# Kernel optimization log

Hardware: AMD Instinct MI355X
Metric: run time of the kernel (lower is better)

Reference implementation:

```python
import jax, jax.numpy as jnp
import numpy as np

HEADS = 8
DIM_HEAD = 32
GROUPS = 8
EPS = 1e-5


def setup_inputs() -> dict:
    key = jax.random.key(0)
    k0, k1, k2 = jax.random.split(key, 3)
    dim = 256
    inner = HEADS * DIM_HEAD  # 256
    x = jax.random.normal(k0, (1, dim, 16, 16, 16), dtype=jnp.float32)
    gn_weight = jnp.ones((dim,), dtype=jnp.float32)
    gn_bias = jnp.zeros((dim,), dtype=jnp.float32)
    w_qkv = jax.random.normal(k1, (3 * inner, dim), dtype=jnp.float32) * 0.02
    w_out = jax.random.normal(k2, (dim, inner), dtype=jnp.float32) * 0.02
    b_out = jnp.zeros((dim,), dtype=jnp.float32)
    return {"x": x, "gn_weight": gn_weight, "gn_bias": gn_bias,
            "w_qkv": w_qkv, "w_out": w_out, "b_out": b_out}


def reference(x, gn_weight, gn_bias, w_qkv, w_out, b_out):
    b, c, d, h, w = x.shape
    n = d * h * w  # tokens

    # --- GroupNorm(8, c) with affine ---
    xg = x.reshape(b, GROUPS, c // GROUPS, n)
    mean = xg.mean(axis=(2, 3), keepdims=True)
    var = xg.var(axis=(2, 3), keepdims=True)
    xn = ((xg - mean) * jax.lax.rsqrt(var + EPS)).reshape(b, c, n)
    xn = xn * gn_weight[:, None] + gn_bias[:, None]

    # --- 1x1 Conv3d QKV projection (no bias) ---
    qkv = jnp.einsum('bcn,oc->bon', xn, w_qkv)              # (b, 3*H*dh, n)
    qkv = qkv.reshape(b, 3, HEADS, DIM_HEAD, n)
    q, k, v = qkv[:, 0], qkv[:, 1], qkv[:, 2]               # each (b, H, dh, n)

    # --- naive softmax attention over n = d*h*w tokens ---
    scale = DIM_HEAD ** (-0.5)
    sim = jnp.einsum('bhdi,bhdj->bhij', q, k) * scale       # (b, H, n, n)
    attn = jax.nn.softmax(sim, axis=-1)
    out = jnp.einsum('bhij,bhdj->bhdi', attn, v)            # (b, H, dh, n)
    out = out.reshape(b, HEADS * DIM_HEAD, n)

    # --- 1x1 Conv3d output projection (with bias) ---
    y = jnp.einsum('bcn,oc->bon', out, w_out) + b_out[:, None]
    return y.reshape(b, c, d, h, w)
```

## Files before the change

### kernel.cpp

```cpp
#include <hip/hip_runtime.h>
#include <hip/hip_bf16.h>
#include <math.h>


typedef __attribute__((ext_vector_type(8))) short bf16x8;
typedef __attribute__((ext_vector_type(4))) short bf16x4;
typedef __attribute__((ext_vector_type(4))) float f32x4;
typedef __attribute__((ext_vector_type(4))) unsigned short u16x4;

__device__ inline unsigned short f2bf(float f) {
  __hip_bfloat16 h = __float2bfloat16(f);
  return *reinterpret_cast<unsigned short*>(&h);
}

__device__ inline bf16x4 pack4_bf(float p0, float p1, float p2, float p3) {
  float2 a, b;
  a.x = p0; a.y = p1; b.x = p2; b.y = p3;
  __hip_bfloat162 lo = __float22bfloat162_rn(a);
  __hip_bfloat162 hi = __float22bfloat162_rn(b);
  union U { __hip_bfloat162 h2[2]; bf16x4 v; } u;
  u.h2[0] = lo; u.h2[1] = hi;
  return u.v;
}

__global__ __launch_bounds__(256) void xt_gn_kernel(const float* __restrict__ x,
                                                    unsigned short* __restrict__ xTb,
                                                    float2* __restrict__ psum2) {
  __shared__ float tile[64][65];
  __shared__ float red[4][4];
  int nb = blockIdx.x * 64, cb = blockIdx.y * 64;
  int tn = threadIdx.x & 63, t4 = threadIdx.x >> 6;
  float slo = 0.f, qlo = 0.f, shi = 0.f, qhi = 0.f;
#pragma unroll
  for (int i = 0; i < 16; ++i) {
    int cc = t4 + i * 4;
    float v = x[(size_t)(cb + cc) * 4096 + nb + tn];
    tile[cc][tn] = v;
    if (i < 8) { slo += v; qlo += v * v; } else { shi += v; qhi += v * v; }
  }
#pragma unroll
  for (int off = 32; off > 0; off >>= 1) {
    slo += __shfl_down(slo, off); qlo += __shfl_down(qlo, off);
    shi += __shfl_down(shi, off); qhi += __shfl_down(qhi, off);
  }
  if ((threadIdx.x & 63) == 0) {
    red[t4][0] = slo; red[t4][1] = qlo; red[t4][2] = shi; red[t4][3] = qhi;
  }
  __syncthreads();
  if (threadIdx.x == 0) {
    float a = (red[0][0] + red[1][0]) + (red[2][0] + red[3][0]);
    float b = (red[0][1] + red[1][1]) + (red[2][1] + red[3][1]);
    psum2[(blockIdx.y * 2) * 64 + blockIdx.x] = make_float2(a, b);
  } else if (threadIdx.x == 64) {
    float a = (red[0][2] + red[1][2]) + (red[2][2] + red[3][2]);
    float b = (red[0][3] + red[1][3]) + (red[2][3] + red[3][3]);
    psum2[(blockIdx.y * 2 + 1) * 64 + blockIdx.x] = make_float2(a, b);
  }
#pragma unroll
  for (int i = 0; i < 16; ++i) {
    int nn = t4 + i * 4;
    xTb[(size_t)(nb + nn) * 256 + cb + tn] = f2bf(tile[tn][nn]);
  }
}

__global__ __launch_bounds__(256) void fold_all_kernel(const float* __restrict__ w_qkv,
                                                       const float* __restrict__ gnw,
                                                       const float* __restrict__ gnb,
                                                       const float2* __restrict__ psum2,
                                                       const float* __restrict__ w_out,
                                                       unsigned short* __restrict__ w2b,
                                                       float* __restrict__ bias0,
                                                       unsigned short* __restrict__ w_outb) {
  int bid = blockIdx.x;
  int t = threadIdx.x;
  if (bid >= 192) {
    int i = ((bid - 192) * 256 + t) * 4;
    float4 v = *(const float4*)(w_out + i);
    u16x4 o;
    o[0] = f2bf(v.x); o[1] = f2bf(v.y); o[2] = f2bf(v.z); o[3] = f2bf(v.w);
    *(u16x4*)(w_outb + i) = o;
    return;
  }
  __shared__ float sm[8], sr[8];
  __shared__ float s_al[256], s_be[256];
  {
    int g = t >> 5, ii = t & 31;
    float2 p0 = psum2[g * 64 + ii];
    float2 p1 = psum2[g * 64 + 32 + ii];
    float s = p0.x + p1.x, q = p0.y + p1.y;
#pragma unroll
    for (int off = 16; off > 0; off >>= 1) {
      s += __shfl_xor(s, off);
      q += __shfl_xor(q, off);
    }
    if (ii == 0) {
      float mean = s * (1.f / 131072.f);
      float var = q * (1.f / 131072.f) - mean * mean;
      sm[g] = mean;
      sr[g] = rsqrtf(var + 1e-5f);
    }
  }
  __syncthreads();
  {
    int c = t, gg = c >> 5;
    float mean = sm[gg], rstd = sr[gg];
    float al = rstd * gnw[c];
    s_al[c] = al;
    s_be[c] = gnb[c] - mean * al;
  }
  __syncthreads();
  int w = t >> 6, lane = t & 63;
  int row = bid * 4 + w;
  float4 v = *(const float4*)(w_qkv + row * 256 + lane * 4);
  int c0 = lane * 4;
  float part = (v.x * s_be[c0] + v.y * s_be[c0 + 1]) +
               (v.z * s_be[c0 + 2] + v.w * s_be[c0 + 3]);
  u16x4 o;
  o[0] = f2bf(v.x * s_al[c0]);
  o[1] = f2bf(v.y * s_al[c0 + 1]);
  o[2] = f2bf(v.z * s_al[c0 + 2]);
  o[3] = f2bf(v.w * s_al[c0 + 3]);
  *(u16x4*)(w2b + row * 256 + c0) = o;
#pragma unroll
  for (int off = 32; off > 0; off >>= 1) part += __shfl_down(part, off);
  if (lane == 0) bias0[row] = part;
}

__global__ __launch_bounds__(256) void gemm_qkv_mfma(const unsigned short* __restrict__ w2b,
                                                     const unsigned short* __restrict__ xTb,
                                                     const float* __restrict__ bias0,
                                                     unsigned short* __restrict__ qt,
                                                     unsigned short* __restrict__ ktb,
                                                     unsigned short* __restrict__ v16) {
  const int nb = blockIdx.x, mb = blockIdx.y;
  const int t = threadIdx.x;
  const int w = t >> 6, lane = t & 63;
  const int c = lane & 15, g = lane >> 4;
  const int m0 = mb * 64 + w * 16;
  const int n0 = nb * 64;
  const f32x4 zero4 = {0.f, 0.f, 0.f, 0.f};

  const unsigned short* ap = w2b + (size_t)(m0 + c) * 256 + g * 8;
  bf16x8 af[8];
#pragma unroll
  for (int ks = 0; ks < 8; ++ks) af[ks] = *(const bf16x8*)(ap + ks * 32);

  f32x4 acc[4] = {zero4, zero4, zero4, zero4};
  const unsigned short* bp = xTb + (size_t)(n0 + c) * 256 + g * 8;
#pragma unroll
  for (int half = 0; half < 2; ++half) {
    bf16x8 bf[4][4];
#pragma unroll
    for (int nt = 0; nt < 4; ++nt)
#pragma unroll
      for (int k2 = 0; k2 < 4; ++k2)
        bf[nt][k2] = *(const bf16x8*)(bp + (size_t)nt * 4096 + half * 128 + k2 * 32);
#pragma unroll
    for (int k2 = 0; k2 < 4; ++k2)
#pragma unroll
      for (int nt = 0; nt < 4; ++nt)
        acc[nt] = __builtin_amdgcn_mfma_f32_16x16x32_bf16(af[half * 4 + k2], bf[nt][k2],
                                                          acc[nt], 0, 0, 0);
  }

  const int o0 = m0 + g * 4;
  const int t3 = o0 >> 8;
  const int h = (o0 >> 5) & 7;
  const int d0 = o0 & 31;
  float b4[4];
#pragma unroll
  for (int r = 0; r < 4; ++r) b4[r] = bias0[o0 + r];
  const float qs = 0.17677669529663687f * 1.4426950408889634f;
#pragma unroll
  for (int nt = 0; nt < 4; ++nt) {
    int n = n0 + nt * 16 + c;
    if (t3 == 0) {
      u16x4 v;
#pragma unroll
      for (int r = 0; r < 4; ++r) v[r] = f2bf((acc[nt][r] + b4[r]) * qs);
      *(u16x4*)(qt + (size_t)(h * 4096 + n) * 32 + d0) = v;
    } else if (t3 == 1) {
      u16x4 v;
#pragma unroll
      for (int r = 0; r < 4; ++r) v[r] = f2bf(acc[nt][r] + b4[r]);
      *(u16x4*)(ktb + (size_t)(h * 4096 + n) * 32 + d0) = v;
    } else {
#pragma unroll
      for (int r = 0; r < 4; ++r)
        v16[(size_t)((h * 256 + (n >> 4)) * 32 + d0 + r) * 16 + (n & 15)] =
            f2bf(acc[nt][r] + b4[r]);
    }
  }
}

__global__ __launch_bounds__(512) void attn_mfma_kernel(const unsigned short* __restrict__ qt,
                                                        const unsigned short* __restrict__ ktb,
                                                        const unsigned short* __restrict__ v16,
                                                        unsigned short* __restrict__ outTb) {
  const int b = blockIdx.x;
  const int h = b & 7;
  const int i0 = (b >> 3) * 64;
  const int t = threadIdx.x;
  const int w = t >> 6;
  const int lane = t & 63;
  const int c = lane & 15;
  const int g = lane >> 4;
  const f32x4 zero4 = {0.f, 0.f, 0.f, 0.f};

  const unsigned short* qb = qt + (size_t)h * 131072 + (size_t)(i0 + c) * 32 + g * 8;
  bf16x8 qf[4];
#pragma unroll
  for (int it = 0; it < 4; ++it) qf[it] = *(const bf16x8*)(qb + it * 512);

  const unsigned short* kp = ktb + (size_t)h * 131072 + (size_t)(w * 512 + c) * 32 + g * 8;
  const unsigned short* vp = v16 + (size_t)((h * 256 + w * 32) * 32 + c) * 16 + g * 4;

  float l[4] = {0.f, 0.f, 0.f, 0.f};
  f32x4 oacc[4][2];
#pragma unroll
  for (int it = 0; it < 4; ++it) {
    oacc[it][0] = zero4;
    oacc[it][1] = zero4;
  }

  bf16x8 kf[4], kn[4];
#pragma unroll
  for (int js = 0; js < 4; ++js) kf[js] = *(const bf16x8*)(kp + js * 512);

#pragma unroll 1
  for (int jt = 0; jt < 8; ++jt) {
    bf16x4 vf[2][4];
#pragma unroll
    for (int dh = 0; dh < 2; ++dh)
#pragma unroll
      for (int js = 0; js < 4; ++js)
        vf[dh][js] = *(const bf16x4*)(vp + (jt * 4 + js) * 512 + dh * 256);
    int jn = (jt < 7) ? jt + 1 : 7;
#pragma unroll
    for (int js = 0; js < 4; ++js)
      kn[js] = *(const bf16x8*)(kp + jn * 2048 + js * 512);

#pragma unroll
    for (int it = 0; it < 4; ++it) {
      f32x4 st[4];
      __builtin_amdgcn_s_setprio(1);
#pragma unroll
      for (int js = 0; js < 4; ++js)
        st[js] = __builtin_amdgcn_mfma_f32_16x16x32_bf16(kf[js], qf[it], zero4, 0, 0, 0);
      __builtin_amdgcn_s_setprio(0);
      bf16x4 pb[4];
      float lsum = 0.f;
#pragma unroll
      for (int js = 0; js < 4; ++js) {
        float p0 = __builtin_amdgcn_exp2f(st[js][0]);
        float p1 = __builtin_amdgcn_exp2f(st[js][1]);
        float p2 = __builtin_amdgcn_exp2f(st[js][2]);
        float p3 = __builtin_amdgcn_exp2f(st[js][3]);
        lsum += (p0 + p1) + (p2 + p3);
        pb[js] = pack4_bf(p0, p1, p2, p3);
      }
      l[it] += lsum;
      __builtin_amdgcn_s_setprio(1);
#pragma unroll
      for (int js = 0; js < 4; ++js) {
        oacc[it][0] = __builtin_amdgcn_mfma_f32_16x16x16bf16_1k(vf[0][js], pb[js], oacc[it][0], 0, 0, 0);
        oacc[it][1] = __builtin_amdgcn_mfma_f32_16x16x16bf16_1k(vf[1][js], pb[js], oacc[it][1], 0, 0, 0);
      }
      __builtin_amdgcn_s_setprio(0);
    }
#pragma unroll
    for (int js = 0; js < 4; ++js) kf[js] = kn[js];
  }

  __shared__ float lds_o[8][4][2][4][4][17];
  __shared__ float lds_l[8][4][16];
#pragma unroll
  for (int it = 0; it < 4; ++it) {
    float lv = l[it];
    lv += __shfl_xor(lv, 16);
    lv += __shfl_xor(lv, 32);
    if (g == 0) lds_l[w][it][c] = lv;
#pragma unroll
    for (int dh = 0; dh < 2; ++dh)
#pragma unroll
      for (int r = 0; r < 4; ++r)
        lds_o[w][it][dh][g][r][c] = oacc[it][dh][r];
  }
  __syncthreads();
  {
    const int it = w & 3;
    const int dh = w >> 2;
    float L = ((lds_l[0][it][c] + lds_l[1][it][c]) + (lds_l[2][it][c] + lds_l[3][it][c])) +
              ((lds_l[4][it][c] + lds_l[5][it][c]) + (lds_l[6][it][c] + lds_l[7][it][c]));
    float inv = 1.f / L;
    u16x4 o;
#pragma unroll
    for (int r = 0; r < 4; ++r) {
      float v = ((lds_o[0][it][dh][g][r][c] + lds_o[1][it][dh][g][r][c]) +
                 (lds_o[2][it][dh][g][r][c] + lds_o[3][it][dh][g][r][c])) +
                ((lds_o[4][it][dh][g][r][c] + lds_o[5][it][dh][g][r][c]) +
                 (lds_o[6][it][dh][g][r][c] + lds_o[7][it][dh][g][r][c]));
      o[r] = f2bf(v * inv);
    }
    *(u16x4*)(outTb + (size_t)(i0 + it * 16 + c) * 256 + h * 32 + dh * 16 + g * 4) = o;
  }
}

__global__ __launch_bounds__(256) void gemm_out_mfma(const unsigned short* __restrict__ w_outb,
                                                     const unsigned short* __restrict__ outTb,
                                                     const float* __restrict__ bias,
                                                     float* __restrict__ y) {
  const int nb = blockIdx.x, mb = blockIdx.y;
  const int t = threadIdx.x;
  const int w = t >> 6, lane = t & 63;
  const int c = lane & 15, g = lane >> 4;
  const int m0 = mb * 64 + w * 16;
  const int n0 = nb * 64;
  const f32x4 zero4 = {0.f, 0.f, 0.f, 0.f};

  const unsigned short* ap = w_outb + (size_t)(m0 + c) * 256 + g * 8;
  bf16x8 af[8];
#pragma unroll
  for (int ks = 0; ks < 8; ++ks) af[ks] = *(const bf16x8*)(ap + ks * 32);

  f32x4 acc[4] = {zero4, zero4, zero4, zero4};
  const unsigned short* bp = outTb + (size_t)(n0 + c) * 256 + g * 8;
#pragma unroll
  for (int half = 0; half < 2; ++half) {
    bf16x8 bf[4][4];
#pragma unroll
    for (int nt = 0; nt < 4; ++nt)
#pragma unroll
      for (int k2 = 0; k2 < 4; ++k2)
        bf[nt][k2] = *(const bf16x8*)(bp + (size_t)nt * 4096 + half * 128 + k2 * 32);
#pragma unroll
    for (int k2 = 0; k2 < 4; ++k2)
#pragma unroll
      for (int nt = 0; nt < 4; ++nt)
        acc[nt] = __builtin_amdgcn_mfma_f32_16x16x32_bf16(af[half * 4 + k2], bf[nt][k2],
                                                          acc[nt], 0, 0, 0);
  }

  const int o0 = m0 + g * 4;
  float b4[4];
#pragma unroll
  for (int r = 0; r < 4; ++r) b4[r] = bias[o0 + r];
#pragma unroll
  for (int nt = 0; nt < 4; ++nt) {
    int n = n0 + nt * 16 + c;
#pragma unroll
    for (int r = 0; r < 4; ++r)
      y[(size_t)(o0 + r) * 4096 + n] = acc[nt][r] + b4[r];
  }
}

extern "C" void kernel_launch(void* const* d_in, const int* in_sizes, int n_in,
                              void* d_out, int out_size, void* d_ws, size_t ws_size,
                              hipStream_t stream) {
  const float* x = (const float*)d_in[0];
  const float* gnw = (const float*)d_in[1];
  const float* gnb = (const float*)d_in[2];
  const float* w_qkv = (const float*)d_in[3];
  const float* w_out = (const float*)d_in[4];
  const float* b_out = (const float*)d_in[5];
  float* ws = (float*)d_ws;

  float2* psum2 = (float2*)ws;
  float* bias0 = ws + 1088;
  unsigned short* w2b = (unsigned short*)(ws + 2048);
  unsigned short* w_outb = w2b + 196608;
  unsigned short* xTb = w_outb + 65536;
  unsigned short* qt = xTb + 1048576;
  unsigned short* ktb = qt + 1048576;
  unsigned short* v16 = ktb + 1048576;
  unsigned short* outTb = v16 + 1048576;
  float* y = (float*)d_out;

  hipLaunchKernelGGL(xt_gn_kernel, dim3(64, 4), dim3(256), 0, stream, x, xTb, psum2);
  hipLaunchKernelGGL(fold_all_kernel, dim3(256), dim3(256), 0, stream, w_qkv, gnw, gnb,
                     psum2, w_out, w2b, bias0, w_outb);
  hipLaunchKernelGGL(gemm_qkv_mfma, dim3(64, 12), dim3(256), 0, stream, w2b, xTb, bias0, qt, ktb, v16);
  hipLaunchKernelGGL(attn_mfma_kernel, dim3(512), dim3(512), 0, stream, qt, ktb, v16, outTb);
  hipLaunchKernelGGL(gemm_out_mfma, dim3(64, 4), dim3(256), 0, stream, w_outb, outTb, b_out, y);
}
```

Measured before the change: 69.78 us.

## Stage K/V tiles in LDS with async double buffering, split attention by queries

The attention kernel now gives each wave its own 16 query rows and has every wave walk all keys. K and V tiles are staged into swizzled LDS double buffers with global_load_lds, so all 8 waves share one copy of each tile instead of each wave loading its own key slice from global memory. This removes the cross-wave LDS reduction of partial outputs and row sums at the end. V is written by the QKV GEMM in a plain transposed [h][d][n] layout to suit the LDS staging. The grid halves to 256 blocks of 128 queries, which lowers parallelism and adds a block barrier per key tile.

After: 82.39 us. 1.18x slower.

```diff
diff --git a/kernel.cpp b/kernel.cpp
--- a/kernel.cpp
+++ b/kernel.cpp
@@ -21,6 +21,12 @@
   union U { __hip_bfloat162 h2[2]; bf16x4 v; } u;
   u.h2[0] = lo; u.h2[1] = hi;
   return u.v;
+}
+
+__device__ inline void gld_lds16(const void* g, void* l) {
+  __builtin_amdgcn_global_load_lds(
+      (const __attribute__((address_space(1))) void*)g,
+      (__attribute__((address_space(3))) void*)l, 16, 0, 0);
 }
 
 __global__ __launch_bounds__(256) void xt_gn_kernel(const float* __restrict__ x,
@@ -131,7 +137,7 @@
                                                      const float* __restrict__ bias0,
                                                      unsigned short* __restrict__ qt,
                                                      unsigned short* __restrict__ ktb,
-                                                     unsigned short* __restrict__ v16) {
+                                                     unsigned short* __restrict__ vT) {
   const int nb = blockIdx.x, mb = blockIdx.y;
   const int t = threadIdx.x;
   const int w = t >> 6, lane = t & 63;
@@ -187,19 +193,18 @@
     } else {
 #pragma unroll
       for (int r = 0; r < 4; ++r)
-        v16[(size_t)((h * 256 + (n >> 4)) * 32 + d0 + r) * 16 + (n & 15)] =
-            f2bf(acc[nt][r] + b4[r]);
+        vT[(size_t)(h * 32 + d0 + r) * 4096 + n] = f2bf(acc[nt][r] + b4[r]);
     }
   }
 }
 
 __global__ __launch_bounds__(512) void attn_mfma_kernel(const unsigned short* __restrict__ qt,
                                                         const unsigned short* __restrict__ ktb,
-                                                        const unsigned short* __restrict__ v16,
+                                                        const unsigned short* __restrict__ vT,
                                                         unsigned short* __restrict__ outTb) {
   const int b = blockIdx.x;
   const int h = b & 7;
-  const int i0 = (b >> 3) * 64;
+  const int i0 = (b >> 3) * 128;
   const int t = threadIdx.x;
   const int w = t >> 6;
   const int lane = t & 63;
@@ -207,102 +212,87 @@
   const int g = lane >> 4;
   const f32x4 zero4 = {0.f, 0.f, 0.f, 0.f};
 
-  const unsigned short* qb = qt + (size_t)h * 131072 + (size_t)(i0 + c) * 32 + g * 8;
-  bf16x8 qf[4];
-#pragma unroll
-  for (int it = 0; it < 4; ++it) qf[it] = *(const bf16x8*)(qb + it * 512);
-
-  const unsigned short* kp = ktb + (size_t)h * 131072 + (size_t)(w * 512 + c) * 32 + g * 8;
-  const unsigned short* vp = v16 + (size_t)((h * 256 + w * 32) * 32 + c) * 16 + g * 4;
-
-  float l[4] = {0.f, 0.f, 0.f, 0.f};
-  f32x4 oacc[4][2];
-#pragma unroll
-  for (int it = 0; it < 4; ++it) {
-    oacc[it][0] = zero4;
-    oacc[it][1] = zero4;
-  }
-
-  bf16x8 kf[4], kn[4];
-#pragma unroll
-  for (int js = 0; js < 4; ++js) kf[js] = *(const bf16x8*)(kp + js * 512);
-
+  __shared__ __align__(16) unsigned short kbuf[2][4096];
+  __shared__ __align__(16) unsigned short vbuf[2][4096];
+
+  const bf16x8 qf = *(const bf16x8*)(qt + (size_t)h * 131072 +
+                                     (size_t)(i0 + w * 16 + c) * 32 + g * 8);
+
+  const char* kbase = (const char*)(ktb + (size_t)h * 131072);
+  const char* vbase = (const char*)(vT + (size_t)h * 131072);
+  const int ksrc = (t * 16) ^ (((t >> 3) & 3) << 4);
+  const int vd = t >> 4;
+  const int vsrc = ((t & 15) * 16) ^ ((vd & 7) << 4);
+  char* kdst0 = (char*)&kbuf[0][0] + w * 1024;
+  char* vdst0 = (char*)&vbuf[0][0] + w * 1024;
+
+  const int krd_base = c * 64 + g * 16;
+  const int kswz = ((c >> 1) & 3) << 4;
+  const int vswz = (c & 7) << 4;
+
+  f32x4 oacc[2] = {zero4, zero4};
+  float l = 0.f;
+
+#define STAGE(bb, tt)                                                     \
+  do {                                                                    \
+    gld_lds16(kbase + (size_t)(tt) * 8192 + ksrc, kdst0 + (bb) * 8192);   \
+    gld_lds16(vbase + (size_t)vd * 8192 + (size_t)(tt) * 256 + vsrc,      \
+              vdst0 + (bb) * 8192);                                       \
+  } while (0)
+
+  STAGE(0, 0);
+  __syncthreads();
+
+  int cur = 0;
 #pragma unroll 1
-  for (int jt = 0; jt < 8; ++jt) {
-    bf16x4 vf[2][4];
+  for (int tt = 0; tt < 32; ++tt) {
+    if (tt < 31) STAGE(cur ^ 1, tt + 1);
+
+    const char* kb = (const char*)&kbuf[cur][0];
+    const char* vb = (const char*)&vbuf[cur][0];
+
+    f32x4 st[8];
+#pragma unroll
+    for (int js = 0; js < 8; ++js) {
+      bf16x8 kf = *(const bf16x8*)(kb + ((js * 1024 + krd_base) ^ kswz));
+      st[js] = __builtin_amdgcn_mfma_f32_16x16x32_bf16(kf, qf, zero4, 0, 0, 0);
+    }
+
+    bf16x4 pb[8];
+    float lsum = 0.f;
+#pragma unroll
+    for (int js = 0; js < 8; ++js) {
+      float p0 = __builtin_amdgcn_exp2f(st[js][0]);
+      float p1 = __builtin_amdgcn_exp2f(st[js][1]);
+      float p2 = __builtin_amdgcn_exp2f(st[js][2]);
+      float p3 = __builtin_amdgcn_exp2f(st[js][3]);
+      lsum += (p0 + p1) + (p2 + p3);
+      pb[js] = pack4_bf(p0, p1, p2, p3);
+    }
+    l += lsum;
+
 #pragma unroll
     for (int dh = 0; dh < 2; ++dh)
 #pragma unroll
-      for (int js = 0; js < 4; ++js)
-        vf[dh][js] = *(const bf16x4*)(vp + (jt * 4 + js) * 512 + dh * 256);
-    int jn = (jt < 7) ? jt + 1 : 7;
-#pragma unroll
-    for (int js = 0; js < 4; ++js)
-      kn[js] = *(const bf16x8*)(kp + jn * 2048 + js * 512);
-
-#pragma unroll
-    for (int it = 0; it < 4; ++it) {
-      f32x4 st[4];
-      __builtin_amdgcn_s_setprio(1);
-#pragma unroll
-      for (int js = 0; js < 4; ++js)
-        st[js] = __builtin_amdgcn_mfma_f32_16x16x32_bf16(kf[js], qf[it], zero4, 0, 0, 0);
-      __builtin_amdgcn_s_setprio(0);
-      bf16x4 pb[4];
-      float lsum = 0.f;
-#pragma unroll
-      for (int js = 0; js < 4; ++js) {
-        float p0 = __builtin_amdgcn_exp2f(st[js][0]);
-        float p1 = __builtin_amdgcn_exp2f(st[js][1]);
-        float p2 = __builtin_amdgcn_exp2f(st[js][2]);
-        float p3 = __builtin_amdgcn_exp2f(st[js][3]);
-        lsum += (p0 + p1) + (p2 + p3);
-        pb[js] = pack4_bf(p0, p1, p2, p3);
+      for (int js = 0; js < 8; ++js) {
+        bf16x4 vf = *(const bf16x4*)(vb + (((dh * 16 + c) * 256 + js * 32 + g * 8) ^ vswz));
+        oacc[dh] = __builtin_amdgcn_mfma_f32_16x16x16bf16_1k(vf, pb[js], oacc[dh], 0, 0, 0);
       }
-      l[it] += lsum;
-      __builtin_amdgcn_s_setprio(1);
-#pragma unroll
-      for (int js = 0; js < 4; ++js) {
-        oacc[it][0] = __builtin_amdgcn_mfma_f32_16x16x16bf16_1k(vf[0][js], pb[js], oacc[it][0], 0, 0, 0);
-        oacc[it][1] = __builtin_amdgcn_mfma_f32_16x16x16bf16_1k(vf[1][js], pb[js], oacc[it][1], 0, 0, 0);
-      }
-      __builtin_amdgcn_s_setprio(0);
-    }
-#pragma unroll
-    for (int js = 0; js < 4; ++js) kf[js] = kn[js];
-  }
-
-  __shared__ float lds_o[8][4][2][4][4][17];
-  __shared__ float lds_l[8][4][16];
-#pragma unroll
-  for (int it = 0; it < 4; ++it) {
-    float lv = l[it];
-    lv += __shfl_xor(lv, 16);
-    lv += __shfl_xor(lv, 32);
-    if (g == 0) lds_l[w][it][c] = lv;
-#pragma unroll
-    for (int dh = 0; dh < 2; ++dh)
-#pragma unroll
-      for (int r = 0; r < 4; ++r)
-        lds_o[w][it][dh][g][r][c] = oacc[it][dh][r];
-  }
-  __syncthreads();
-  {
-    const int it = w & 3;
-    const int dh = w >> 2;
-    float L = ((lds_l[0][it][c] + lds_l[1][it][c]) + (lds_l[2][it][c] + lds_l[3][it][c])) +
-              ((lds_l[4][it][c] + lds_l[5][it][c]) + (lds_l[6][it][c] + lds_l[7][it][c]));
-    float inv = 1.f / L;
+
+    __syncthreads();
+    cur ^= 1;
+  }
+#undef STAGE
+
+  l += __shfl_xor(l, 16);
+  l += __shfl_xor(l, 32);
+  float inv = 1.f / l;
+#pragma unroll
+  for (int dh = 0; dh < 2; ++dh) {
     u16x4 o;
 #pragma unroll
-    for (int r = 0; r < 4; ++r) {
-      float v = ((lds_o[0][it][dh][g][r][c] + lds_o[1][it][dh][g][r][c]) +
-                 (lds_o[2][it][dh][g][r][c] + lds_o[3][it][dh][g][r][c])) +
-                ((lds_o[4][it][dh][g][r][c] + lds_o[5][it][dh][g][r][c]) +
-                 (lds_o[6][it][dh][g][r][c] + lds_o[7][it][dh][g][r][c]));
-      o[r] = f2bf(v * inv);
-    }
-    *(u16x4*)(outTb + (size_t)(i0 + it * 16 + c) * 256 + h * 32 + dh * 16 + g * 4) = o;
+    for (int r = 0; r < 4; ++r) o[r] = f2bf(oacc[dh][r] * inv);
+    *(u16x4*)(outTb + (size_t)(i0 + w * 16 + c) * 256 + h * 32 + dh * 16 + g * 4) = o;
   }
 }
 
@@ -372,14 +362,14 @@
   unsigned short* xTb = w_outb + 65536;
   unsigned short* qt = xTb + 1048576;
   unsigned short* ktb = qt + 1048576;
-  unsigned short* v16 = ktb + 1048576;
-  unsigned short* outTb = v16 + 1048576;
+  unsigned short* vT = ktb + 1048576;
+  unsigned short* outTb = vT + 1048576;
   float* y = (float*)d_out;
 
   hipLaunchKernelGGL(xt_gn_kernel, dim3(64, 4), dim3(256), 0, stream, x, xTb, psum2);
   hipLaunchKernelGGL(fold_all_kernel, dim3(256), dim3(256), 0, stream, w_qkv, gnw, gnb,
                      psum2, w_out, w2b, bias0, w_outb);
-  hipLaunchKernelGGL(gemm_qkv_mfma, dim3(64, 12), dim3(256), 0, stream, w2b, xTb, bias0, qt, ktb, v16);
-  hipLaunchKernelGGL(attn_mfma_kernel, dim3(512), dim3(512), 0, stream, qt, ktb, v16, outTb);
+  hipLaunchKernelGGL(gemm_qkv_mfma, dim3(64, 12), dim3(256), 0, stream, w2b, xTb, bias0, qt, ktb, vT);
+  hipLaunchKernelGGL(attn_mfma_kernel, dim3(256), dim3(512), 0, stream, qt, ktb, vT, outTb);
   hipLaunchKernelGGL(gemm_out_mfma, dim3(64, 4), dim3(256), 0, stream, w_outb, outTb, b_out, y);
 }
```
